# Optimization experiments

Hardware: AMD Instinct MI355X
Metric: run time of the kernel (lower is better)

The kernel has to match this reference:

```python
import jax, jax.numpy as jnp
import numpy as np

B = 65536          # number of 9-node graphs
NPG = 9            # nodes per graph (hardcoded in module)
N = B * NPG
D_IN, D_H = 11, 64
SOFTPLUS_BIAS = float(np.log(np.expm1(1.0)))  # biased_softplus_1.0 bias
SCALE_LB = 1e-4


def _make_edges():
    # fully connected (no self loops) within each 9-node graph
    pairs = np.array([(i, j) for i in range(NPG) for j in range(NPG) if i != j],
                     dtype=np.int64)  # [72, 2]
    offs = (np.arange(B, dtype=np.int64) * NPG)[:, None]
    src = (offs + pairs[None, :, 0]).ravel()
    dst = (offs + pairs[None, :, 1]).ravel()
    return jnp.asarray(np.stack([src, dst]))  # [2, E]


def setup_inputs() -> dict:
    key = jax.random.key(0)
    ks = jax.random.split(key, 12)
    s_in = 1.0 / np.sqrt(D_IN)
    s_h = 1.0 / np.sqrt(D_H)
    return {
        "x": jax.random.normal(ks[0], (N, D_IN), jnp.float32),
        "edge_index": _make_edges(),
        "W_in": jax.random.normal(ks[1], (D_H, D_IN), jnp.float32) * s_in,
        "b_in": jax.random.normal(ks[2], (D_H,), jnp.float32) * s_in,
        "W1_rel": jax.random.normal(ks[3], (D_H, D_H), jnp.float32) * s_h,
        "b1": jax.random.normal(ks[4], (D_H,), jnp.float32) * s_h,
        "W1_root": jax.random.normal(ks[5], (D_H, D_H), jnp.float32) * s_h,
        "W2_rel": jax.random.normal(ks[6], (D_H, D_H), jnp.float32) * s_h,
        "b2": jax.random.normal(ks[7], (D_H,), jnp.float32) * s_h,
        "W2_root": jax.random.normal(ks[8], (D_H, D_H), jnp.float32) * s_h,
        "W_head": jax.random.normal(ks[9], (8, D_H, 2), jnp.float32) * s_h,
        "b_head": jax.random.normal(ks[10], (8, 2), jnp.float32) * s_h,
    }


def _graph_conv(x, src, dst, W_rel, b_rel, W_root, n):
    # PyG GraphConv: lin_rel(sum_{j in N(i)} x_j) + lin_root(x_i)
    agg = jax.ops.segment_sum(x[src], dst, num_segments=n)  # scatter-add gather
    return agg @ W_rel.T + b_rel + x @ W_root.T


def reference(x, edge_index, W_in, b_in, W1_rel, b1, W1_root,
              W2_rel, b2, W2_root, W_head, b_head):
    n = x.shape[0]
    src, dst = edge_index[0], edge_index[1]
    h = x @ W_in.T + b_in                                   # [N, 64]
    h = jnp.tanh(_graph_conv(h, src, dst, W1_rel, b1, W1_root, n))
    h = jnp.tanh(_graph_conv(h, src, dst, W2_rel, b2, W2_root, n))
    hg = h.reshape(n // NPG, NPG, D_H)[:, 1:, :]            # drop node 0: [B, 8, 64]
    out = jnp.einsum('bnd,ndo->bno', hg, W_head) + b_head   # per-node head: [B, 8, 2]
    loc = out[..., 0]
    scale = jnp.maximum(jax.nn.softplus(out[..., 1] + SOFTPLUS_BIAS), SCALE_LB)
    return (loc, scale)
```

## Files before the change

### kernel.cpp

```cpp
#include <hip/hip_runtime.h>
#include <hip/hip_bf16.h>

#define NPG 9
#define DH 64
#define DIN 11
#define GPB 28
#define ROWS (GPB*NPG)
#define TPB 256
#define NGRAPH 65536
#define NROWTOT (NGRAPH*NPG)
#define NBLK ((NGRAPH + GPB - 1)/GPB)
#define OUT_HALF ((long long)NGRAPH*8)

typedef __attribute__((ext_vector_type(8))) short short8;
typedef __attribute__((ext_vector_type(4))) short short4v;
typedef __attribute__((ext_vector_type(4))) float f32x4;

__device__ float g_c1[DH];
__device__ short g_bfrag1[4*512];
__device__ short g_bfrag2[16*512];
__device__ short g_bfragH[2*512];

__device__ __forceinline__ short f2bs(float f) {
  __hip_bfloat16 h = __float2bfloat16(f);
  return __builtin_bit_cast(short, h);
}
__device__ __forceinline__ float b2f(short s) {
  unsigned u = ((unsigned)(unsigned short)s) << 16;
  return __builtin_bit_cast(float, u);
}
__device__ __forceinline__ float fast_tanh(float v) {
  float e = __expf(2.f*v);
  return 1.f - 2.f*__builtin_amdgcn_rcpf(e + 1.f);
}

__global__ void prep_kernel(const float* __restrict__ W_in, const float* __restrict__ b_in,
                            const float* __restrict__ W1_rel, const float* __restrict__ b1,
                            const float* __restrict__ W1_root,
                            const float* __restrict__ W2_rel, const float* __restrict__ W2_root,
                            const float* __restrict__ W_head) {
  __shared__ float Wa[DH][DIN+1], Wb[DH][DIN+1];
  const int tid = threadIdx.x;
  for (int t = tid; t < DH*DIN; t += 1024) {
    int n = t / DIN, k = t - n*DIN;
    float a = 0.f, b = 0.f;
    for (int m = 0; m < DH; ++m) {
      float wi = W_in[m*DIN + k];
      float r  = W1_rel[n*DH + m];
      a += (W1_root[n*DH + m] - r) * wi;
      b += r * wi;
    }
    Wa[n][k] = a; Wb[n][k] = b;
  }
  if (tid < DH) {
    float c = b1[tid];
    for (int m = 0; m < DH; ++m)
      c += (W1_root[tid*DH + m] + 8.f*W1_rel[tid*DH + m]) * b_in[m];
    g_c1[tid] = c;
  }
  __syncthreads();
  for (int i = tid; i < 4*512; i += 1024) {
    int nt = i >> 9;
    int l = (i >> 3) & 63, j = i & 7;
    int k = ((l >> 4) << 3) + j;
    int n = nt*16 + (l & 15);
    float v = 0.f;
    if (k < 16) { if (k < DIN) v = Wa[n][k]; }
    else        { if (k - 16 < DIN) v = Wb[n][k - 16]; }
    g_bfrag1[i] = f2bs(v);
  }
  for (int i = tid; i < 16*512; i += 1024) {
    int frag = i >> 9, kk = frag >> 2, nt = frag & 3;
    int l = (i >> 3) & 63, j = i & 7;
    int k2 = kk*32 + ((l >> 4) << 3) + j;
    int n  = nt*16 + (l & 15);
    float v = (k2 < 64) ? (W2_root[n*DH + k2] - W2_rel[n*DH + k2])
                        : W2_rel[n*DH + k2 - 64];
    g_bfrag2[i] = f2bs(v);
  }
  for (int i = tid; i < 2*512; i += 1024) {
    int kk = i >> 9;
    int l = (i >> 3) & 63, j = i & 7;
    int k = kk*32 + ((l >> 4) << 3) + j;
    int n = l & 15;
    g_bfragH[i] = f2bs(W_head[(n >> 1)*(DH*2) + k*2 + (n & 1)]);
  }
}

#define HS_W(r, col) ((r)*64 + (((((col) >> 3)) ^ ((r) & 7)) << 3) + ((col) & 7))
#define HS_CH(r, c)  ((r)*64 + (((c) ^ ((r) & 7)) << 3))

__global__ __launch_bounds__(TPB, 4) void fused_kernel(
    const float* __restrict__ x,
    const float* __restrict__ b2,
    const float* __restrict__ bhead,
    float* __restrict__ out)
{
  __shared__ short Hs[ROWS*DH];
  __shared__ union {
    struct { short xs[ROWS*12]; short Sx[GPB*12]; } a;
    short ss[GPB*64];
  } U;

  const int tid  = threadIdx.x;
  const int lane = tid & 63;
  const int wave = tid >> 6;
  const int l15  = lane & 15;
  const int kgrp = lane >> 4;

  short* xs = U.a.xs;
  short* Sx = U.a.Sx;
  short* ss = U.ss;

  {
    const long long base = (long long)blockIdx.x * (ROWS*DIN);
    long long rem = (long long)NROWTOT*DIN - base;
    const int lim = rem < (ROWS*DIN) ? (int)rem : (ROWS*DIN);
    for (int i = tid; i < lim; i += TPB) {
      int r = (int)(((unsigned)i * 2979u) >> 15);
      int c = i - r*DIN;
      xs[r*12 + c] = f2bs(x[base + i]);
    }
    if (tid < ROWS) xs[tid*12 + 11] = 0;
  }
  __syncthreads();

  if (tid < GPB*2) {
    const int g = tid >> 1, half = tid & 1;
    const int rbase = g*NPG;
    float s[8] = {0,0,0,0,0,0,0,0};
    for (int j = 0; j < NPG; ++j) {
      const short* p = &xs[(rbase + j)*12 + half*8];
      short4v a = *(const short4v*)p;
      short4v b = *(const short4v*)(p + 4);
      s[0] += b2f(a[0]); s[1] += b2f(a[1]); s[2] += b2f(a[2]); s[3] += b2f(a[3]);
      s[4] += b2f(b[0]); s[5] += b2f(b[1]); s[6] += b2f(b[2]); s[7] += b2f(b[3]);
    }
    short4v o0;
    o0[0] = f2bs(s[0]); o0[1] = f2bs(s[1]); o0[2] = f2bs(s[2]); o0[3] = f2bs(s[3]);
    *(short4v*)&Sx[g*12 + half*8] = o0;
    if (!half) {
      short4v o1;
      o1[0] = f2bs(s[4]); o1[1] = f2bs(s[5]); o1[2] = f2bs(s[6]); o1[3] = f2bs(s[7]);
      *(short4v*)&Sx[g*12 + 4] = o1;
    }
  }
  __syncthreads();

  {
    short8 B1[4];
    #pragma unroll
    for (int nt = 0; nt < 4; ++nt) B1[nt] = *(const short8*)&g_bfrag1[nt*512 + lane*8];
    float c1v[4];
    #pragma unroll
    for (int nt = 0; nt < 4; ++nt) c1v[nt] = g_c1[nt*16 + l15];

    const int sel = kgrp & 1;
    #pragma unroll
    for (int i = 0; i < 4; ++i) {
      const int t = wave*4 + i;
      int row = t*16 + l15; if (row > ROWS-1) row = ROWS-1;
      const int g = (row*57) >> 9;
      const short* bp = (kgrp < 2) ? &xs[row*12] : &Sx[g*12];
      short4v lo = *(const short4v*)(bp + sel*8);
      short4v hi = *(const short4v*)(bp + 4);
      short8 A;
      A[0] = lo[0]; A[1] = lo[1]; A[2] = lo[2]; A[3] = lo[3];
      A[4] = sel ? (short)0 : hi[0];
      A[5] = sel ? (short)0 : hi[1];
      A[6] = sel ? (short)0 : hi[2];
      A[7] = sel ? (short)0 : hi[3];
      f32x4 acc[4];
      #pragma unroll
      for (int nt = 0; nt < 4; ++nt)
        acc[nt] = (f32x4){c1v[nt], c1v[nt], c1v[nt], c1v[nt]};
      #pragma unroll
      for (int nt = 0; nt < 4; ++nt)
        acc[nt] = __builtin_amdgcn_mfma_f32_16x16x32_bf16(A, B1[nt], acc[nt], 0, 0, 0);
      #pragma unroll
      for (int nt = 0; nt < 4; ++nt) {
        #pragma unroll
        for (int reg = 0; reg < 4; ++reg) {
          const int orow = t*16 + kgrp*4 + reg;
          if (orow < ROWS) {
            const int col = nt*16 + l15;
            Hs[HS_W(orow, col)] = f2bs(fast_tanh(acc[nt][reg]));
          }
        }
      }
    }
  }
  __syncthreads();

  if (tid < GPB*8) {
    const int fc = (int)(((unsigned)tid * 2341u) >> 16);
    const int g  = tid - fc*GPB;
    float s[8] = {0,0,0,0,0,0,0,0};
    for (int j = 0; j < NPG; ++j) {
      const int r = g*NPG + j;
      short8 v = *(const short8*)&Hs[HS_CH(r, fc)];
      #pragma unroll
      for (int e = 0; e < 8; ++e) s[e] += b2f(v[e]);
    }
    short8 o;
    #pragma unroll
    for (int e = 0; e < 8; ++e) o[e] = f2bs(s[e]);
    *(short8*)&ss[g*64 + ((fc ^ (g & 7)) << 3)] = o;
  }
  __syncthreads();

  {
    short8 B2[4][4];
    #pragma unroll
    for (int kk = 0; kk < 4; ++kk)
      #pragma unroll
      for (int nt = 0; nt < 4; ++nt)
        B2[kk][nt] = *(const short8*)&g_bfrag2[((kk << 2) + nt)*512 + lane*8];
    float b2v[4];
    #pragma unroll
    for (int nt = 0; nt < 4; ++nt) b2v[nt] = b2[nt*16 + l15];

    #pragma unroll
    for (int i = 0; i < 4; ++i) {
      const int t = wave*4 + i;
      int row = t*16 + l15; if (row > ROWS-1) row = ROWS-1;
      const int g = (row*57) >> 9;
      short8 A[4];
      A[0] = *(const short8*)&Hs[HS_CH(row, 0 + kgrp)];
      A[1] = *(const short8*)&Hs[HS_CH(row, 4 + kgrp)];
      A[2] = *(const short8*)&ss[g*64 + (((0 + kgrp) ^ (g & 7)) << 3)];
      A[3] = *(const short8*)&ss[g*64 + (((4 + kgrp) ^ (g & 7)) << 3)];
      f32x4 acc[4];
      #pragma unroll
      for (int nt = 0; nt < 4; ++nt)
        acc[nt] = (f32x4){b2v[nt], b2v[nt], b2v[nt], b2v[nt]};
      #pragma unroll
      for (int kk = 0; kk < 4; ++kk)
        #pragma unroll
        for (int nt = 0; nt < 4; ++nt)
          acc[nt] = __builtin_amdgcn_mfma_f32_16x16x32_bf16(A[kk], B2[kk][nt], acc[nt], 0, 0, 0);
      #pragma unroll
      for (int nt = 0; nt < 4; ++nt) {
        #pragma unroll
        for (int reg = 0; reg < 4; ++reg) {
          const int orow = t*16 + kgrp*4 + reg;
          if (orow < ROWS) {
            const int col = nt*16 + l15;
            Hs[HS_W(orow, col)] = f2bs(fast_tanh(acc[nt][reg]));
          }
        }
      }
    }
  }
  __syncthreads();

  {
    short8 HB0 = *(const short8*)&g_bfragH[lane*8];
    short8 HB1 = *(const short8*)&g_bfragH[512 + lane*8];
    const int p  = l15 >> 1;
    const int oc = l15 & 1;
    const float bh = bhead[p*2 + oc];
    #pragma unroll
    for (int i = 0; i < 4; ++i) {
      const int t = wave*4 + i;
      int row = t*16 + l15; if (row > ROWS-1) row = ROWS-1;
      short8 A0 = *(const short8*)&Hs[HS_CH(row, 0 + kgrp)];
      short8 A1 = *(const short8*)&Hs[HS_CH(row, 4 + kgrp)];
      f32x4 acc = (f32x4){bh, bh, bh, bh};
      acc = __builtin_amdgcn_mfma_f32_16x16x32_bf16(A0, HB0, acc, 0, 0, 0);
      acc = __builtin_amdgcn_mfma_f32_16x16x32_bf16(A1, HB1, acc, 0, 0, 0);
      #pragma unroll
      for (int reg = 0; reg < 4; ++reg) {
        const int orow = t*16 + kgrp*4 + reg;
        if (orow < ROWS) {
          const int g  = (orow*57) >> 9;
          const int nn = orow - g*NPG;
          const long long gg = (long long)blockIdx.x*GPB + g;
          if (nn == p + 1 && gg < NGRAPH) {
            const float v = acc[reg];
            if (oc == 0) {
              out[gg*8 + p] = v;
            } else {
              float tv = v + 0.5413248546129181f;
              float e  = __expf(tv);
              float sp = (tv > 15.f) ? tv : __logf(1.f + e);
              out[OUT_HALF + gg*8 + p] = fmaxf(sp, 1e-4f);
            }
          }
        }
      }
    }
  }
}

extern "C" void kernel_launch(void* const* d_in, const int* in_sizes, int n_in,
                              void* d_out, int out_size, void* d_ws, size_t ws_size,
                              hipStream_t stream) {
  const float* x       = (const float*)d_in[0];
  const float* W_in    = (const float*)d_in[2];
  const float* b_in    = (const float*)d_in[3];
  const float* W1_rel  = (const float*)d_in[4];
  const float* b1      = (const float*)d_in[5];
  const float* W1_root = (const float*)d_in[6];
  const float* W2_rel  = (const float*)d_in[7];
  const float* b2      = (const float*)d_in[8];
  const float* W2_root = (const float*)d_in[9];
  const float* Whead   = (const float*)d_in[10];
  const float* bhead   = (const float*)d_in[11];
  float* out = (float*)d_out;

  hipLaunchKernelGGL(prep_kernel, dim3(1), dim3(1024), 0, stream,
                     W_in, b_in, W1_rel, b1, W1_root, W2_rel, W2_root, Whead);
  hipLaunchKernelGGL(fused_kernel, dim3(NBLK), dim3(TPB), 0, stream,
                     x, b2, bhead, out);
}
```

Before: 226.7 us.

## Map one graph per 16-row MFMA tile, wave-local pipeline without block barriers

```diff
diff --git a/kernel.cpp b/kernel.cpp
--- a/kernel.cpp
+++ b/kernel.cpp
@@ -4,30 +4,25 @@
 #define NPG 9
 #define DH 64
 #define DIN 11
-#define GPB 28
-#define ROWS (GPB*NPG)
+#define GPB 16
+#define TPW 4
 #define TPB 256
 #define NGRAPH 65536
-#define NROWTOT (NGRAPH*NPG)
-#define NBLK ((NGRAPH + GPB - 1)/GPB)
+#define NBLK (NGRAPH/GPB)
+#define XTOT (NGRAPH*NPG*DIN)
 #define OUT_HALF ((long long)NGRAPH*8)
 
 typedef __attribute__((ext_vector_type(8))) short short8;
-typedef __attribute__((ext_vector_type(4))) short short4v;
 typedef __attribute__((ext_vector_type(4))) float f32x4;
 
 __device__ float g_c1[DH];
-__device__ short g_bfrag1[4*512];
+__device__ short g_bfrag1[8*512];
 __device__ short g_bfrag2[16*512];
 __device__ short g_bfragH[2*512];
 
 __device__ __forceinline__ short f2bs(float f) {
   __hip_bfloat16 h = __float2bfloat16(f);
   return __builtin_bit_cast(short, h);
-}
-__device__ __forceinline__ float b2f(short s) {
-  unsigned u = ((unsigned)(unsigned short)s) << 16;
-  return __builtin_bit_cast(float, u);
 }
 __device__ __forceinline__ float fast_tanh(float v) {
   float e = __expf(2.f*v);
@@ -39,56 +34,49 @@
                             const float* __restrict__ W1_root,
                             const float* __restrict__ W2_rel, const float* __restrict__ W2_root,
                             const float* __restrict__ W_head) {
-  __shared__ float Wa[DH][DIN+1], Wb[DH][DIN+1];
-  const int tid = threadIdx.x;
-  for (int t = tid; t < DH*DIN; t += 1024) {
-    int n = t / DIN, k = t - n*DIN;
-    float a = 0.f, b = 0.f;
-    for (int m = 0; m < DH; ++m) {
-      float wi = W_in[m*DIN + k];
-      float r  = W1_rel[n*DH + m];
-      a += (W1_root[n*DH + m] - r) * wi;
-      b += r * wi;
-    }
-    Wa[n][k] = a; Wb[n][k] = b;
-  }
-  if (tid < DH) {
-    float c = b1[tid];
-    for (int m = 0; m < DH; ++m)
-      c += (W1_root[tid*DH + m] + 8.f*W1_rel[tid*DH + m]) * b_in[m];
-    g_c1[tid] = c;
-  }
-  __syncthreads();
-  for (int i = tid; i < 4*512; i += 1024) {
-    int nt = i >> 9;
-    int l = (i >> 3) & 63, j = i & 7;
-    int k = ((l >> 4) << 3) + j;
-    int n = nt*16 + (l & 15);
-    float v = 0.f;
-    if (k < 16) { if (k < DIN) v = Wa[n][k]; }
-    else        { if (k - 16 < DIN) v = Wb[n][k - 16]; }
-    g_bfrag1[i] = f2bs(v);
-  }
-  for (int i = tid; i < 16*512; i += 1024) {
-    int frag = i >> 9, kk = frag >> 2, nt = frag & 3;
-    int l = (i >> 3) & 63, j = i & 7;
-    int k2 = kk*32 + ((l >> 4) << 3) + j;
-    int n  = nt*16 + (l & 15);
-    float v = (k2 < 64) ? (W2_root[n*DH + k2] - W2_rel[n*DH + k2])
-                        : W2_rel[n*DH + k2 - 64];
-    g_bfrag2[i] = f2bs(v);
-  }
-  for (int i = tid; i < 2*512; i += 1024) {
-    int kk = i >> 9;
-    int l = (i >> 3) & 63, j = i & 7;
-    int k = kk*32 + ((l >> 4) << 3) + j;
-    int n = l & 15;
-    g_bfragH[i] = f2bs(W_head[(n >> 1)*(DH*2) + k*2 + (n & 1)]);
-  }
-}
-
-#define HS_W(r, col) ((r)*64 + (((((col) >> 3)) ^ ((r) & 7)) << 3) + ((col) & 7))
-#define HS_CH(r, c)  ((r)*64 + (((c) ^ ((r) & 7)) << 3))
+  const int blk = blockIdx.x, tid = threadIdx.x;
+  if (blk < 2) {
+    for (int i = blk*256 + tid; i < 8*512; i += 512) {
+      int f = i >> 9, l = (i >> 3) & 63, j = i & 7;
+      int k = ((l >> 4) << 3) + j;
+      int n = ((f & 3) << 4) + (l & 15);
+      float v = 0.f;
+      if (k < DIN) {
+        for (int m = 0; m < DH; ++m) {
+          float wi = W_in[m*DIN + k];
+          float r  = W1_rel[n*DH + m];
+          v += ((f < 4) ? (W1_root[n*DH + m] - r) : r) * wi;
+        }
+      }
+      g_bfrag1[i] = f2bs(v);
+    }
+  } else if (blk < 10) {
+    for (int i = (blk - 2)*256 + tid; i < 16*512; i += 2048) {
+      int frag = i >> 9, kk = frag >> 2;
+      int l = (i >> 3) & 63, j = i & 7;
+      int k2 = kk*32 + ((l >> 4) << 3) + j;
+      int n  = (frag & 3)*16 + (l & 15);
+      float v = (k2 < 64) ? (W2_root[n*DH + k2] - W2_rel[n*DH + k2])
+                          : W2_rel[n*DH + k2 - 64];
+      g_bfrag2[i] = f2bs(v);
+    }
+  } else if (blk == 10) {
+    for (int i = tid; i < 2*512; i += 256) {
+      int kk = i >> 9;
+      int l = (i >> 3) & 63, j = i & 7;
+      int k = kk*32 + ((l >> 4) << 3) + j;
+      int n = l & 15;
+      g_bfragH[i] = f2bs(W_head[(n >> 1)*(DH*2) + k*2 + (n & 1)]);
+    }
+  } else {
+    if (tid < DH) {
+      float c = b1[tid];
+      for (int m = 0; m < DH; ++m)
+        c += (W1_root[tid*DH + m] + 8.f*W1_rel[tid*DH + m]) * b_in[m];
+      g_c1[tid] = c;
+    }
+  }
+}
 
 __global__ __launch_bounds__(TPB, 4) void fused_kernel(
     const float* __restrict__ x,
@@ -96,118 +84,91 @@
     const float* __restrict__ bhead,
     float* __restrict__ out)
 {
-  __shared__ short Hs[ROWS*DH];
-  __shared__ union {
-    struct { short xs[ROWS*12]; short Sx[GPB*12]; } a;
-    short ss[GPB*64];
-  } U;
+  __shared__ short Hs[256*64];
+  __shared__ short Ss[GPB*64];
 
   const int tid  = threadIdx.x;
   const int lane = tid & 63;
   const int wave = tid >> 6;
   const int l15  = lane & 15;
   const int kgrp = lane >> 4;
-
-  short* xs = U.a.xs;
-  short* Sx = U.a.Sx;
-  short* ss = U.ss;
+  const int ksel = kgrp & 1;
+  const int t0   = wave*TPW;
+  const unsigned gg0 = (unsigned)blockIdx.x*GPB + t0;
 
   {
-    const long long base = (long long)blockIdx.x * (ROWS*DIN);
-    long long rem = (long long)NROWTOT*DIN - base;
-    const int lim = rem < (ROWS*DIN) ? (int)rem : (ROWS*DIN);
-    for (int i = tid; i < lim; i += TPB) {
-      int r = (int)(((unsigned)i * 2979u) >> 15);
-      int c = i - r*DIN;
-      xs[r*12 + c] = f2bs(x[base + i]);
-    }
-    if (tid < ROWS) xs[tid*12 + 11] = 0;
-  }
-  __syncthreads();
-
-  if (tid < GPB*2) {
-    const int g = tid >> 1, half = tid & 1;
-    const int rbase = g*NPG;
-    float s[8] = {0,0,0,0,0,0,0,0};
-    for (int j = 0; j < NPG; ++j) {
-      const short* p = &xs[(rbase + j)*12 + half*8];
-      short4v a = *(const short4v*)p;
-      short4v b = *(const short4v*)(p + 4);
-      s[0] += b2f(a[0]); s[1] += b2f(a[1]); s[2] += b2f(a[2]); s[3] += b2f(a[3]);
-      s[4] += b2f(b[0]); s[5] += b2f(b[1]); s[6] += b2f(b[2]); s[7] += b2f(b[3]);
-    }
-    short4v o0;
-    o0[0] = f2bs(s[0]); o0[1] = f2bs(s[1]); o0[2] = f2bs(s[2]); o0[3] = f2bs(s[3]);
-    *(short4v*)&Sx[g*12 + half*8] = o0;
-    if (!half) {
-      short4v o1;
-      o1[0] = f2bs(s[4]); o1[1] = f2bs(s[5]); o1[2] = f2bs(s[6]); o1[3] = f2bs(s[7]);
-      *(short4v*)&Sx[g*12 + 4] = o1;
-    }
-  }
-  __syncthreads();
-
-  {
-    short8 B1[4];
-    #pragma unroll
-    for (int nt = 0; nt < 4; ++nt) B1[nt] = *(const short8*)&g_bfrag1[nt*512 + lane*8];
+    short8 By[4], Bu[4];
+    #pragma unroll
+    for (int nt = 0; nt < 4; ++nt) {
+      By[nt] = *(const short8*)&g_bfrag1[nt*512 + lane*8];
+      Bu[nt] = *(const short8*)&g_bfrag1[(4 + nt)*512 + lane*8];
+    }
     float c1v[4];
     #pragma unroll
     for (int nt = 0; nt < 4; ++nt) c1v[nt] = g_c1[nt*16 + l15];
 
-    const int sel = kgrp & 1;
-    #pragma unroll
-    for (int i = 0; i < 4; ++i) {
-      const int t = wave*4 + i;
-      int row = t*16 + l15; if (row > ROWS-1) row = ROWS-1;
-      const int g = (row*57) >> 9;
-      const short* bp = (kgrp < 2) ? &xs[row*12] : &Sx[g*12];
-      short4v lo = *(const short4v*)(bp + sel*8);
-      short4v hi = *(const short4v*)(bp + 4);
+    float xr[TPW][8];
+    #pragma unroll
+    for (int i = 0; i < TPW; ++i) {
+      const unsigned base = ((gg0 + i)*NPG + l15)*DIN + ksel*8;
+      #pragma unroll
+      for (int j = 0; j < 8; ++j) {
+        const unsigned e = base + j;
+        xr[i][j] = (e < (unsigned)XTOT) ? x[e] : 0.f;
+      }
+    }
+
+    const bool real = (l15 <= 8);
+    #pragma unroll
+    for (int i = 0; i < TPW; ++i) {
+      const int T = t0 + i;
       short8 A;
-      A[0] = lo[0]; A[1] = lo[1]; A[2] = lo[2]; A[3] = lo[3];
-      A[4] = sel ? (short)0 : hi[0];
-      A[5] = sel ? (short)0 : hi[1];
-      A[6] = sel ? (short)0 : hi[2];
-      A[7] = sel ? (short)0 : hi[3];
-      f32x4 acc[4];
-      #pragma unroll
-      for (int nt = 0; nt < 4; ++nt)
-        acc[nt] = (f32x4){c1v[nt], c1v[nt], c1v[nt], c1v[nt]};
-      #pragma unroll
-      for (int nt = 0; nt < 4; ++nt)
-        acc[nt] = __builtin_amdgcn_mfma_f32_16x16x32_bf16(A, B1[nt], acc[nt], 0, 0, 0);
-      #pragma unroll
-      for (int nt = 0; nt < 4; ++nt) {
+      #pragma unroll
+      for (int j = 0; j < 8; ++j) {
+        bool ok = real && (ksel == 0 || j < 3);
+        A[j] = ok ? f2bs(xr[i][j]) : (short)0;
+      }
+      f32x4 y[4], u[4];
+      #pragma unroll
+      for (int nt = 0; nt < 4; ++nt) { y[nt] = (f32x4){0,0,0,0}; u[nt] = (f32x4){0,0,0,0}; }
+      #pragma unroll
+      for (int nt = 0; nt < 4; ++nt) {
+        y[nt] = __builtin_amdgcn_mfma_f32_16x16x32_bf16(A, By[nt], y[nt], 0, 0, 0);
+        u[nt] = __builtin_amdgcn_mfma_f32_16x16x32_bf16(A, Bu[nt], u[nt], 0, 0, 0);
+      }
+      float suc[4];
+      #pragma unroll
+      for (int nt = 0; nt < 4; ++nt) {
+        float s = (u[nt][0] + u[nt][1]) + (u[nt][2] + u[nt][3]);
+        s += __shfl_xor(s, 16);
+        s += __shfl_xor(s, 32);
+        suc[nt] = s + c1v[nt];
+      }
+      float sh[4];
+      #pragma unroll
+      for (int nt = 0; nt < 4; ++nt) {
+        float acc = 0.f;
         #pragma unroll
         for (int reg = 0; reg < 4; ++reg) {
-          const int orow = t*16 + kgrp*4 + reg;
-          if (orow < ROWS) {
-            const int col = nt*16 + l15;
-            Hs[HS_W(orow, col)] = f2bs(fast_tanh(acc[nt][reg]));
-          }
+          const int row = kgrp*4 + reg;
+          float v = fast_tanh(y[nt][reg] + suc[nt]);
+          v = (row <= 8) ? v : 0.f;
+          acc += v;
+          const int rr  = T*16 + row;
+          const int col = nt*16 + l15;
+          Hs[rr*64 + ((((col >> 3) ^ (row & 7))) << 3) + (col & 7)] = f2bs(v);
         }
-      }
-    }
-  }
-  __syncthreads();
-
-  if (tid < GPB*8) {
-    const int fc = (int)(((unsigned)tid * 2341u) >> 16);
-    const int g  = tid - fc*GPB;
-    float s[8] = {0,0,0,0,0,0,0,0};
-    for (int j = 0; j < NPG; ++j) {
-      const int r = g*NPG + j;
-      short8 v = *(const short8*)&Hs[HS_CH(r, fc)];
-      #pragma unroll
-      for (int e = 0; e < 8; ++e) s[e] += b2f(v[e]);
-    }
-    short8 o;
-    #pragma unroll
-    for (int e = 0; e < 8; ++e) o[e] = f2bs(s[e]);
-    *(short8*)&ss[g*64 + ((fc ^ (g & 7)) << 3)] = o;
-  }
-  __syncthreads();
+        sh[nt] = acc;
+      }
+      #pragma unroll
+      for (int nt = 0; nt < 4; ++nt) {
+        float s = sh[nt];
+        s += __shfl_xor(s, 16);
+        s += __shfl_xor(s, 32);
+        if (kgrp == 0) Ss[T*64 + nt*16 + l15] = f2bs(s);
+      }
+    }
+  }
 
   {
     short8 B2[4][4];
@@ -215,79 +176,74 @@
     for (int kk = 0; kk < 4; ++kk)
       #pragma unroll
       for (int nt = 0; nt < 4; ++nt)
-        B2[kk][nt] = *(const short8*)&g_bfrag2[((kk << 2) + nt)*512 + lane*8];
+        B2[kk][nt] = *(const short8*)&g_bfrag2[(kk*4 + nt)*512 + lane*8];
     float b2v[4];
     #pragma unroll
     for (int nt = 0; nt < 4; ++nt) b2v[nt] = b2[nt*16 + l15];
 
     #pragma unroll
-    for (int i = 0; i < 4; ++i) {
-      const int t = wave*4 + i;
-      int row = t*16 + l15; if (row > ROWS-1) row = ROWS-1;
-      const int g = (row*57) >> 9;
-      short8 A[4];
-      A[0] = *(const short8*)&Hs[HS_CH(row, 0 + kgrp)];
-      A[1] = *(const short8*)&Hs[HS_CH(row, 4 + kgrp)];
-      A[2] = *(const short8*)&ss[g*64 + (((0 + kgrp) ^ (g & 7)) << 3)];
-      A[3] = *(const short8*)&ss[g*64 + (((4 + kgrp) ^ (g & 7)) << 3)];
+    for (int i = 0; i < TPW; ++i) {
+      const int T = t0 + i;
+      const int row = T*16 + l15;
+      short8 A0 = *(const short8*)&Hs[row*64 + (((0 + kgrp) ^ (l15 & 7)) << 3)];
+      short8 A1 = *(const short8*)&Hs[row*64 + (((4 + kgrp) ^ (l15 & 7)) << 3)];
+      short8 A2 = *(const short8*)&Ss[T*64 + kgrp*8];
+      short8 A3 = *(const short8*)&Ss[T*64 + 32 + kgrp*8];
       f32x4 acc[4];
       #pragma unroll
       for (int nt = 0; nt < 4; ++nt)
         acc[nt] = (f32x4){b2v[nt], b2v[nt], b2v[nt], b2v[nt]};
       #pragma unroll
-      for (int kk = 0; kk < 4; ++kk)
-        #pragma unroll
-        for (int nt = 0; nt < 4; ++nt)
-          acc[nt] = __builtin_amdgcn_mfma_f32_16x16x32_bf16(A[kk], B2[kk][nt], acc[nt], 0, 0, 0);
+      for (int nt = 0; nt < 4; ++nt) {
+        acc[nt] = __builtin_amdgcn_mfma_f32_16x16x32_bf16(A0, B2[0][nt], acc[nt], 0, 0, 0);
+        acc[nt] = __builtin_amdgcn_mfma_f32_16x16x32_bf16(A1, B2[1][nt], acc[nt], 0, 0, 0);
+        acc[nt] = __builtin_amdgcn_mfma_f32_16x16x32_bf16(A2, B2[2][nt], acc[nt], 0, 0, 0);
+        acc[nt] = __builtin_amdgcn_mfma_f32_16x16x32_bf16(A3, B2[3][nt], acc[nt], 0, 0, 0);
+      }
       #pragma unroll
       for (int nt = 0; nt < 4; ++nt) {
         #pragma unroll
         for (int reg = 0; reg < 4; ++reg) {
-          const int orow = t*16 + kgrp*4 + reg;
-          if (orow < ROWS) {
-            const int col = nt*16 + l15;
-            Hs[HS_W(orow, col)] = f2bs(fast_tanh(acc[nt][reg]));
-          }
+          const int row2 = kgrp*4 + reg;
+          float v = fast_tanh(acc[nt][reg]);
+          v = (row2 <= 8) ? v : 0.f;
+          const int rr  = T*16 + row2;
+          const int col = nt*16 + l15;
+          Hs[rr*64 + ((((col >> 3) ^ (row2 & 7))) << 3) + (col & 7)] = f2bs(v);
         }
       }
     }
   }
-  __syncthreads();
 
   {
-    short8 HB0 = *(const short8*)&g_bfragH[lane*8];
-    short8 HB1 = *(const short8*)&g_bfragH[512 + lane*8];
+    short8 H0 = *(const short8*)&g_bfragH[lane*8];
+    short8 H1 = *(const short8*)&g_bfragH[512 + lane*8];
     const int p  = l15 >> 1;
     const int oc = l15 & 1;
-    const float bh = bhead[p*2 + oc];
-    #pragma unroll
-    for (int i = 0; i < 4; ++i) {
-      const int t = wave*4 + i;
-      int row = t*16 + l15; if (row > ROWS-1) row = ROWS-1;
-      short8 A0 = *(const short8*)&Hs[HS_CH(row, 0 + kgrp)];
-      short8 A1 = *(const short8*)&Hs[HS_CH(row, 4 + kgrp)];
+    const float bh = bhead[l15];
+    const int trow = p + 1;
+    const bool mykg = ((trow >> 2) == kgrp);
+    const int treg = trow & 3;
+
+    #pragma unroll
+    for (int i = 0; i < TPW; ++i) {
+      const int T = t0 + i;
+      const int row = T*16 + l15;
+      short8 A0 = *(const short8*)&Hs[row*64 + (((0 + kgrp) ^ (l15 & 7)) << 3)];
+      short8 A1 = *(const short8*)&Hs[row*64 + (((4 + kgrp) ^ (l15 & 7)) << 3)];
       f32x4 acc = (f32x4){bh, bh, bh, bh};
-      acc = __builtin_amdgcn_mfma_f32_16x16x32_bf16(A0, HB0, acc, 0, 0, 0);
-      acc = __builtin_amdgcn_mfma_f32_16x16x32_bf16(A1, HB1, acc, 0, 0, 0);
-      #pragma unroll
-      for (int reg = 0; reg < 4; ++reg) {
-        const int orow = t*16 + kgrp*4 + reg;
-        if (orow < ROWS) {
-          const int g  = (orow*57) >> 9;
-          const int nn = orow - g*NPG;
-          const long long gg = (long long)blockIdx.x*GPB + g;
-          if (nn == p + 1 && gg < NGRAPH) {
-            const float v = acc[reg];
-            if (oc == 0) {
-              out[gg*8 + p] = v;
-            } else {
-              float tv = v + 0.5413248546129181f;
-              float e  = __expf(tv);
-              float sp = (tv > 15.f) ? tv : __logf(1.f + e);
-              out[OUT_HALF + gg*8 + p] = fmaxf(sp, 1e-4f);
-            }
-          }
-        }
+      acc = __builtin_amdgcn_mfma_f32_16x16x32_bf16(A0, H0, acc, 0, 0, 0);
+      acc = __builtin_amdgcn_mfma_f32_16x16x32_bf16(A1, H1, acc, 0, 0, 0);
+      float val = (treg & 2) ? ((treg & 1) ? acc[3] : acc[2])
+                             : ((treg & 1) ? acc[1] : acc[0]);
+      float tv = val + 0.5413248546129181f;
+      float e  = __expf(tv);
+      float sp = (tv > 15.f) ? tv : __logf(1.f + e);
+      sp = fmaxf(sp, 1e-4f);
+      float res = oc ? sp : val;
+      if (mykg) {
+        const long long gg = (long long)blockIdx.x*GPB + T;
+        out[(oc ? OUT_HALF : 0) + gg*8 + p] = res;
       }
     }
   }
@@ -309,7 +265,7 @@
   const float* bhead   = (const float*)d_in[11];
   float* out = (float*)d_out;
 
-  hipLaunchKernelGGL(prep_kernel, dim3(1), dim3(1024), 0, stream,
+  hipLaunchKernelGGL(prep_kernel, dim3(12), dim3(256), 0, stream,
                      W_in, b_in, W1_rel, b1, W1_root, W2_rel, W2_root, Whead);
   hipLaunchKernelGGL(fused_kernel, dim3(NBLK), dim3(TPB), 0, stream,
                      x, b2, bhead, out);
```

Result: slower. 295.2 us (+30.2%).
